# Kernel optimization log

Hardware: AMD Instinct MI355X
Metric: run time of the kernel (lower is better)

## Reference

```python
import jax, jax.numpy as jnp
import numpy as np

LAM = 5.0
NUM_STEPS = 100
B, N, D = 16, 1024, 256


def l2_normalize(x, eps=1e-12):
    # tf.math.l2_normalize: x * rsqrt(max(sum(x^2), eps))
    sq = jnp.sum(x * x, axis=-1, keepdims=True)
    return x * jax.lax.rsqrt(jnp.maximum(sq, eps))


def normalize_pij(P):
    return P / jnp.sum(P, axis=(1, 2), keepdims=True)


def sinkhorn_step(P):
    # a_vec = b_vec = ones(N), so u = 1/col_sum, v = 1/row_sum
    P = P / jnp.sum(P, axis=2, keepdims=True)   # scale rows
    P = P / jnp.sum(P, axis=1, keepdims=True)   # scale cols
    return P


def setup_inputs() -> dict:
    key = jax.random.key(0)
    kA, kB = jax.random.split(key)
    fA = jax.random.normal(kA, (B, N, D), dtype=jnp.float32)
    fB = jax.random.normal(kB, (B, N, D), dtype=jnp.float32)
    return {"fA": fA, "fB": fB}


def reference(fA, fB):
    fA = l2_normalize(fA)
    fB = l2_normalize(fB)
    Sij = jnp.einsum("bnd,bmd->bnm", fA, fB)          # [B, N, N]
    Cij = jnp.clip(-Sij, -15.0 / LAM, 15.0 / LAM)

    # batch_compute_optimal_transport
    P = jnp.exp(-LAM * Cij)
    P = normalize_pij(P)

    def step(P, _):
        return sinkhorn_step(P), None

    P, _ = jax.lax.scan(step, P, None, length=NUM_STEPS)

    # straight-through style re-parameterization
    alpha_beta = jax.lax.stop_gradient(P * jnp.exp(LAM * Cij))
    P0 = alpha_beta * jnp.exp(-LAM * Cij)
    P0 = normalize_pij(P0)
    P_out = sinkhorn_step(P0)
    return (P_out, Sij)
```

## Files before the change

kernel.cpp:

```cpp
#include <hip/hip_runtime.h>
#include <stdint.h>

#define NB 16
#define NN 1024
#define ND 256

typedef __bf16 bf16x8 __attribute__((ext_vector_type(8)));
typedef float f32x4 __attribute__((ext_vector_type(4)));

__device__ __forceinline__ unsigned short f2bf(float x){
  unsigned u = __builtin_bit_cast(unsigned, x);
  u += 0x7FFFu + ((u >> 16) & 1u);
  return (unsigned short)(u >> 16);
}
__device__ __forceinline__ float bflo(unsigned u){ return __builtin_bit_cast(float, u << 16); }
__device__ __forceinline__ float bfhi(unsigned u){ return __builtin_bit_cast(float, u & 0xFFFF0000u); }

__global__ __launch_bounds__(256) void norm_cast_kernel(
    const float* __restrict__ fA, const float* __restrict__ fB,
    unsigned short* __restrict__ Abf, unsigned short* __restrict__ Bbf)
{
  int task = blockIdx.x * 4 + (threadIdx.x >> 6);
  int lane = threadIdx.x & 63;
  const float* src = (task < NB*NN) ? fA : fB;
  unsigned short* dst = (task < NB*NN) ? Abf : Bbf;
  int row = (task < NB*NN) ? task : task - NB*NN;
  float4 x = ((const float4*)(src + (size_t)row*ND))[lane];
  float sq = x.x*x.x + x.y*x.y + x.z*x.z + x.w*x.w;
  #pragma unroll
  for (int off = 32; off > 0; off >>= 1) sq += __shfl_xor(sq, off);
  float s = rsqrtf(fmaxf(sq, 1e-12f));
  ushort4 o;
  o.x = f2bf(x.x*s); o.y = f2bf(x.y*s); o.z = f2bf(x.z*s); o.w = f2bf(x.w*s);
  ((ushort4*)(dst + (size_t)row*ND))[lane] = o;
}

#define LDK 40

__global__ __launch_bounds__(256) void gemm_exp_kernel(
    const unsigned short* __restrict__ Abf, const unsigned short* __restrict__ Bbf,
    float* __restrict__ S, unsigned short* __restrict__ Kg)
{
  __shared__ __align__(16) unsigned short As[128*LDK];
  __shared__ __align__(16) unsigned short Bs[128*LDK];
  const int b = blockIdx.z;
  const int mbase = blockIdx.y * 128;
  const int nbase = blockIdx.x * 128;
  const int t = threadIdx.x;
  const int lane = t & 63;
  const int wave = t >> 6;
  const int wm = wave >> 1, wn = wave & 1;
  const int quad = lane >> 4, l16 = lane & 15;

  const unsigned short* Ab = Abf + (size_t)b*NN*ND;
  const unsigned short* Bb = Bbf + (size_t)b*NN*ND;

  f32x4 acc[4][4];
  #pragma unroll
  for (int i=0;i<4;i++)
    #pragma unroll
    for (int j=0;j<4;j++) acc[i][j] = (f32x4){0.f,0.f,0.f,0.f};

  for (int k0 = 0; k0 < ND; k0 += 32){
    __syncthreads();
    #pragma unroll
    for (int i=0;i<2;i++){
      int chunk = t + 256*i;
      int row = chunk >> 2, seg = chunk & 3;
      *(uint4*)(&As[row*LDK + seg*8]) = *(const uint4*)(Ab + (size_t)(mbase+row)*ND + k0 + seg*8);
      *(uint4*)(&Bs[row*LDK + seg*8]) = *(const uint4*)(Bb + (size_t)(nbase+row)*ND + k0 + seg*8);
    }
    __syncthreads();
    bf16x8 af[4], bg[4];
    #pragma unroll
    for (int i=0;i<4;i++){
      af[i] = *(const bf16x8*)(&As[(wm*64 + i*16 + l16)*LDK + quad*8]);
      bg[i] = *(const bf16x8*)(&Bs[(wn*64 + i*16 + l16)*LDK + quad*8]);
    }
    #pragma unroll
    for (int i=0;i<4;i++)
      #pragma unroll
      for (int j=0;j<4;j++)
        acc[i][j] = __builtin_amdgcn_mfma_f32_16x16x32_bf16(af[i], bg[j], acc[i][j], 0, 0, 0);
  }

  float* Sb = S + (size_t)b*NN*NN;
  unsigned short* Kb = Kg + (size_t)b*NN*NN;
  #pragma unroll
  for (int i=0;i<4;i++){
    #pragma unroll
    for (int j=0;j<4;j++){
      int n = nbase + wn*64 + j*16 + l16;
      #pragma unroll
      for (int v=0;v<4;v++){
        int m = mbase + wm*64 + i*16 + quad*4 + v;
        float sv = acc[i][j][v];
        Sb[(size_t)m*NN + n] = sv;
        float sc = fminf(fmaxf(sv, -3.f), 3.f);
        Kb[(size_t)m*NN + n] = f2bf(__expf(5.f*sc));
      }
    }
  }
}

__global__ __launch_bounds__(1024) void sinkhorn_kernel(
    const unsigned short* __restrict__ Kg, float* __restrict__ P,
    float* __restrict__ vsum, unsigned* __restrict__ arrive)
{
  __shared__ __align__(16) float v[NN];
  __shared__ __align__(16) float part[NN];
  __shared__ __align__(16) float u[64];

  const int blk = blockIdx.x;
  const int b = blk >> 4;
  const int rb = blk & 15;
  const int t = threadIdx.x;
  const int w = t >> 6;
  const int l = t & 63;

  const unsigned short* Kgb = Kg + ((size_t)(b*NN + rb*64))*NN;

  unsigned kcol[32];
  #pragma unroll
  for (int k=0;k<32;k++){
    unsigned lo = Kgb[(size_t)(2*k)*NN + t];
    unsigned hi = Kgb[(size_t)(2*k+1)*NN + t];
    kcol[k] = lo | (hi << 16);
  }
  unsigned krow[32];
  {
    const uint4* rs = (const uint4*)(Kgb + (size_t)l*NN + w*64);
    #pragma unroll
    for (int k=0;k<8;k++){
      uint4 q4 = rs[k];
      krow[4*k+0]=q4.x; krow[4*k+1]=q4.y; krow[4*k+2]=q4.z; krow[4*k+3]=q4.w;
    }
  }
  v[t] = 1.0f;
  __syncthreads();

  const float4* v4 = (const float4*)v;
  const float4* u4 = (const float4*)u;
  float* vs_b = vsum + (size_t)b*3*NN;
  unsigned* arr = arrive + b*64;

  int buf = 0;
  for (int it = 0; it < 101; it++){
    float rsum = 0.f;
    #pragma unroll
    for (int k=0;k<16;k++){
      float4 vv = v4[w*16 + k];
      unsigned ka = krow[2*k], kb = krow[2*k+1];
      rsum += bflo(ka)*vv.x + bfhi(ka)*vv.y + bflo(kb)*vv.z + bfhi(kb)*vv.w;
    }
    part[w*64 + l] = rsum;
    __syncthreads();
    if (t < 64){
      float s = 0.f;
      #pragma unroll
      for (int q=0;q<16;q++) s += part[q*64 + t];
      u[t] = 1.0f / s;
    }
    __syncthreads();
    float csum = 0.f;
    #pragma unroll
    for (int k=0;k<16;k++){
      float4 uu = u4[k];
      unsigned ka = kcol[2*k], kb = kcol[2*k+1];
      csum += bflo(ka)*uu.x + bfhi(ka)*uu.y + bflo(kb)*uu.z + bfhi(kb)*uu.w;
    }
    __hip_atomic_fetch_add(vs_b + (size_t)buf*NN + t, csum,
                           __ATOMIC_RELAXED, __HIP_MEMORY_SCOPE_AGENT);
    __syncthreads();
    if (t == 0){
      __hip_atomic_fetch_add(arr, 1u, __ATOMIC_ACQ_REL, __HIP_MEMORY_SCOPE_AGENT);
      unsigned tgt = 16u*(unsigned)(it+1);
      while (__hip_atomic_load(arr, __ATOMIC_ACQUIRE, __HIP_MEMORY_SCOPE_AGENT) < tgt)
        __builtin_amdgcn_s_sleep(1);
    }
    __syncthreads();
    if (it > 0 && t < 64){
      int prevbuf = (buf + 2) % 3;
      __hip_atomic_store(vs_b + (size_t)prevbuf*NN + rb*64 + t, 0.f,
                         __ATOMIC_RELAXED, __HIP_MEMORY_SCOPE_AGENT);
    }
    float cs = __hip_atomic_load(vs_b + (size_t)buf*NN + t,
                                 __ATOMIC_RELAXED, __HIP_MEMORY_SCOPE_AGENT);
    v[t] = 1.0f / cs;
    buf = (buf == 2) ? 0 : buf + 1;
    __syncthreads();
  }

  float* Pb = P + ((size_t)(b*NN + rb*64))*NN;
  float vt = v[t];
  #pragma unroll
  for (int k=0;k<16;k++){
    float4 uu = u4[k];
    unsigned ka = kcol[2*k], kb = kcol[2*k+1];
    Pb[(size_t)(4*k+0)*NN + t] = bflo(ka)*uu.x*vt;
    Pb[(size_t)(4*k+1)*NN + t] = bfhi(ka)*uu.y*vt;
    Pb[(size_t)(4*k+2)*NN + t] = bflo(kb)*uu.z*vt;
    Pb[(size_t)(4*k+3)*NN + t] = bfhi(kb)*uu.w*vt;
  }
}

extern "C" void kernel_launch(void* const* d_in, const int* in_sizes, int n_in,
                              void* d_out, int out_size, void* d_ws, size_t ws_size,
                              hipStream_t stream)
{
  const float* fA = (const float*)d_in[0];
  const float* fB = (const float*)d_in[1];
  float* Pout = (float*)d_out;
  float* Sout = Pout + (size_t)NB*NN*NN;
  unsigned short* Kg = (unsigned short*)d_out;

  unsigned short* Abf = (unsigned short*)d_ws;
  unsigned short* Bbf = Abf + (size_t)NB*NN*ND;
  float* vsum = (float*)((char*)d_ws + (size_t)16*1024*1024);
  unsigned* arrive = (unsigned*)(vsum + (size_t)NB*3*NN);

  hipMemsetAsync(vsum, 0, (size_t)NB*3*NN*4 + (size_t)NB*64*4, stream);
  norm_cast_kernel<<<dim3(8192), dim3(256), 0, stream>>>(fA, fB, Abf, Bbf);
  gemm_exp_kernel<<<dim3(8,8,NB), dim3(256), 0, stream>>>(Abf, Bbf, Sout, Kg);
  sinkhorn_kernel<<<dim3(256), dim3(1024), 0, stream>>>(Kg, Pout, vsum, arrive);
}
```

Measured before the change: 1.664 ms.

## Replace atomic-add plus arrival counter barrier with per-block slot polling

Each of the 16 row-blocks of a batch now writes its column partial sums to its own slot. Every thread polls all 16 slots until they are nonzero and sums them locally, which removes the atomic float adds, the counter barrier and two block-wide syncs per iteration. Block indexing is also permuted so consecutive blocks belong to different batches. The trade-off is 16 loads per thread per poll and reliance on partial sums never being exactly zero to detect readiness.

```diff
diff --git a/kernel.cpp b/kernel.cpp
--- a/kernel.cpp
+++ b/kernel.cpp
@@ -105,15 +105,15 @@
 
 __global__ __launch_bounds__(1024) void sinkhorn_kernel(
     const unsigned short* __restrict__ Kg, float* __restrict__ P,
-    float* __restrict__ vsum, unsigned* __restrict__ arrive)
+    float* __restrict__ slots)
 {
   __shared__ __align__(16) float v[NN];
   __shared__ __align__(16) float part[NN];
   __shared__ __align__(16) float u[64];
 
   const int blk = blockIdx.x;
-  const int b = blk >> 4;
-  const int rb = blk & 15;
+  const int b  = blk & 15;
+  const int rb = blk >> 4;
   const int t = threadIdx.x;
   const int w = t >> 6;
   const int l = t & 63;
@@ -141,10 +141,11 @@
 
   const float4* v4 = (const float4*)v;
   const float4* u4 = (const float4*)u;
-  float* vs_b = vsum + (size_t)b*3*NN;
-  unsigned* arr = arrive + b*64;
+  float* sl_b = slots + (size_t)b*3*16*NN;
+  float* my_slot = sl_b + (size_t)rb*NN + t;
 
   int buf = 0;
+  float vt = 1.0f;
   for (int it = 0; it < 101; it++){
     float rsum = 0.f;
     #pragma unroll
@@ -169,30 +170,32 @@
       unsigned ka = kcol[2*k], kb = kcol[2*k+1];
       csum += bflo(ka)*uu.x + bfhi(ka)*uu.y + bflo(kb)*uu.z + bfhi(kb)*uu.w;
     }
-    __hip_atomic_fetch_add(vs_b + (size_t)buf*NN + t, csum,
-                           __ATOMIC_RELAXED, __HIP_MEMORY_SCOPE_AGENT);
-    __syncthreads();
-    if (t == 0){
-      __hip_atomic_fetch_add(arr, 1u, __ATOMIC_ACQ_REL, __HIP_MEMORY_SCOPE_AGENT);
-      unsigned tgt = 16u*(unsigned)(it+1);
-      while (__hip_atomic_load(arr, __ATOMIC_ACQUIRE, __HIP_MEMORY_SCOPE_AGENT) < tgt)
-        __builtin_amdgcn_s_sleep(1);
-    }
-    __syncthreads();
-    if (it > 0 && t < 64){
-      int prevbuf = (buf + 2) % 3;
-      __hip_atomic_store(vs_b + (size_t)prevbuf*NN + rb*64 + t, 0.f,
-                         __ATOMIC_RELAXED, __HIP_MEMORY_SCOPE_AGENT);
-    }
-    float cs = __hip_atomic_load(vs_b + (size_t)buf*NN + t,
-                                 __ATOMIC_RELAXED, __HIP_MEMORY_SCOPE_AGENT);
-    v[t] = 1.0f / cs;
+    __hip_atomic_store(my_slot + (size_t)buf*16*NN, csum,
+                       __ATOMIC_RELAXED, __HIP_MEMORY_SCOPE_AGENT);
+    const float* base = sl_b + (size_t)buf*16*NN + t;
+    float cs;
+    for (;;){
+      float s0 = 0.f; bool ok = true;
+      #pragma unroll
+      for (int p=0;p<16;p++){
+        float x = __hip_atomic_load(base + (size_t)p*NN,
+                                    __ATOMIC_RELAXED, __HIP_MEMORY_SCOPE_AGENT);
+        ok &= (x != 0.f);
+        s0 += x;
+      }
+      if (ok){ cs = s0; break; }
+      __builtin_amdgcn_s_sleep(1);
+    }
+    int prev = (buf == 0) ? 2 : buf - 1;
+    __hip_atomic_store(my_slot + (size_t)prev*16*NN, 0.f,
+                       __ATOMIC_RELAXED, __HIP_MEMORY_SCOPE_AGENT);
+    vt = 1.0f / cs;
+    v[t] = vt;
     buf = (buf == 2) ? 0 : buf + 1;
     __syncthreads();
   }
 
   float* Pb = P + ((size_t)(b*NN + rb*64))*NN;
-  float vt = v[t];
   #pragma unroll
   for (int k=0;k<16;k++){
     float4 uu = u4[k];
@@ -216,11 +219,10 @@
 
   unsigned short* Abf = (unsigned short*)d_ws;
   unsigned short* Bbf = Abf + (size_t)NB*NN*ND;
-  float* vsum = (float*)((char*)d_ws + (size_t)16*1024*1024);
-  unsigned* arrive = (unsigned*)(vsum + (size_t)NB*3*NN);
-
-  hipMemsetAsync(vsum, 0, (size_t)NB*3*NN*4 + (size_t)NB*64*4, stream);
+  float* slots = (float*)((char*)d_ws + (size_t)16*1024*1024);
+
+  hipMemsetAsync(slots, 0, (size_t)NB*3*16*NN*4, stream);
   norm_cast_kernel<<<dim3(8192), dim3(256), 0, stream>>>(fA, fB, Abf, Bbf);
   gemm_exp_kernel<<<dim3(8,8,NB), dim3(256), 0, stream>>>(Abf, Bbf, Sout, Kg);
-  sinkhorn_kernel<<<dim3(256), dim3(1024), 0, stream>>>(Kg, Pout, vsum, arrive);
-}
+  sinkhorn_kernel<<<dim3(256), dim3(1024), 0, stream>>>(Kg, Pout, slots);
+}
```

Measured after the change: 1.742 ms. 4.7% more time.
